# Kernel optimization log

Hardware: AMD Instinct MI355X
Metric: run time of the kernel (lower is better)

## Reference

```python
import jax, jax.numpy as jnp
from jax import lax
import numpy as np

B, CIN, NC, H, W = 8, 64, 4, 192, 192
TAU = 4.0
ALPHA = 2.0
LOSS_W = 0.5
OVERALL_W = 1.0
K = 3  # edge-extraction kernel size


def setup_inputs() -> dict:
    key = jax.random.key(0)
    k1, k2, k3, k4 = jax.random.split(key, 4)
    feat_student = jax.random.normal(k1, (B, CIN, H, W), jnp.float32)
    logits_teacher = jax.random.normal(k2, (B, NC, H, W), jnp.float32)
    lbl_idx = jax.random.randint(k3, (B, H, W), 0, NC)
    label = jax.nn.one_hot(lbl_idx, NC, axis=1, dtype=jnp.float32)  # (B,NC,H,W)
    # 1x1 conv projector params (kaiming fan_out-ish scale), bias zero-init per module
    W_proj = jax.random.normal(k4, (NC, CIN), jnp.float32) * (2.0 / CIN) ** 0.5
    b_proj = jnp.zeros((NC,), jnp.float32)
    return {"feat_student": feat_student, "logits_teacher": logits_teacher,
            "label": label, "W_proj": W_proj, "b_proj": b_proj}


def _edt(mask):
    """Exact Euclidean distance transform of a bool (H,W) mask: distance of each
    pixel to the nearest False pixel (0 at False pixels). Separable exact EDT:
    1D row distances, then min over rows of f^2 + dr^2."""
    h, w = mask.shape
    big = jnp.float32(h + w)  # > max possible true distance
    pos = jnp.arange(w, dtype=jnp.float32)
    zero = ~mask
    left = lax.cummax(jnp.where(zero, pos, -big), axis=1)            # nearest zero idx to the left
    right = lax.cummin(jnp.where(zero, pos, 2.0 * big), axis=1, reverse=True)
    f = jnp.minimum(jnp.minimum(pos - left, right - pos), big)       # (H,W) 1D row distance
    rr = jnp.arange(h, dtype=jnp.float32)
    dr2 = (rr[:, None] - rr[None, :]) ** 2                           # (H,H)
    d2 = jnp.min(f[None, :, :] ** 2 + dr2[:, :, None], axis=1)       # (H,W)
    return jnp.sqrt(d2)


def _distance_field(img):
    """img: (B,H,W) float. fg_dist + bg_dist per image; zeros if mask all-same
    (mirrors scipy distance_transform_edt loop)."""
    mask = img > 0.5

    def per_image(m):
        nontrivial = m.any() & ~m.all()
        return jnp.where(nontrivial, _edt(m) + _edt(~m), 0.0)

    return jax.vmap(per_image)(mask)


def _extract_edge(label):
    # per-channel 3x3 ones conv == sum pooling; edge where 0 < sum < K*K
    conv = lax.reduce_window(label, 0.0, lax.add, (1, 1, K, K), (1, 1, 1, 1),
                             [(0, 0), (0, 0), (K // 2, K // 2), (K // 2, K // 2)])
    return ((conv > 0) & (conv < K * K)).astype(jnp.float32)


def reference(feat_student, logits_teacher, label, W_proj, b_proj):
    # projector: 1x1 conv
    logits_s = jnp.einsum('bchw,kc->bkhw', feat_student, W_proj) + b_proj[None, :, None, None]

    # ---- BoundaryKD (ECKD) ----
    edge = _extract_edge(label)[:, 1:]              # drop background channel
    s = (logits_s[:, 1:] * edge) / TAU
    t = (logits_teacher[:, 1:] * edge) / TAU
    p = jax.nn.log_softmax(s, axis=1)
    q = jax.nn.softmax(t, axis=1)
    # F.kl_div(p, q, 'batchmean') = sum(q*(log q - p)) / B
    kl = jnp.sum(jax.scipy.special.xlogy(q, q) - q * p) / B
    bkd_loss = kl * TAU ** 2

    # ---- LogHausdorffDT (SRKD) ----
    probs = jax.nn.softmax(logits_s, axis=1)
    tgt = jax.nn.one_hot(jnp.argmax(logits_teacher, axis=1), NC, axis=1, dtype=probs.dtype)
    pf = probs[:, 1:]   # (B, NC-1, H, W)
    tf = tgt[:, 1:]
    losses = []
    for c in range(NC - 1):   # small fixed loop over foreground classes
        pdt = lax.stop_gradient(_distance_field(pf[:, c]))
        tdt = lax.stop_gradient(_distance_field(tf[:, c]))
        err = (pf[:, c] - tf[:, c]) ** 2
        losses.append(jnp.mean(err * (pdt ** ALPHA + tdt ** ALPHA)))
    hd_loss = jnp.log(jnp.mean(jnp.stack(losses)) + 1.0)

    return (bkd_loss * OVERALL_W * LOSS_W, hd_loss * OVERALL_W * (1.0 - LOSS_W))
```

## Files before the change

### kernel.cpp

```cpp
#include <hip/hip_runtime.h>
#include <math.h>

#define BB 8
#define HH 192
#define WW 192
#define HW (HH*WW)
#define NPIX (BB*HW)

#define WS_ERR_OFF   256
#define WS_MP_OFF    3539200
#define WS_MT_OFF    4423936
#define WS_FQ_OFF    5308672

typedef unsigned char  u8;
typedef unsigned short u16;

__global__ __launch_bounds__(256) void k_main(
    const float* __restrict__ feat, const float* __restrict__ teach,
    const float* __restrict__ label, const float* __restrict__ Wp,
    const float* __restrict__ bp,
    float* __restrict__ err, u8* __restrict__ mp, u8* __restrict__ mt,
    int* __restrict__ cntp, int* __restrict__ cntt,
    double* __restrict__ klsum)
{
    __shared__ float  Ws[256];
    __shared__ float  bs[4];
    __shared__ int    scp[3], sct[3];
    __shared__ double skl[4];
    const int tid = threadIdx.x;
    Ws[tid] = Wp[tid];
    if (tid < 4) bs[tid] = bp[tid];
    if (tid < 3) { scp[tid] = 0; sct[tid] = 0; }
    __syncthreads();

    const int pix0 = (blockIdx.x*256 + tid)*2;
    const int b    = pix0 / HW;
    const int rem  = pix0 - b*HW;
    const int h    = rem / WW;
    const int w    = rem - h*WW;

    float acc[4][2];
    #pragma unroll
    for (int k = 0; k < 4; ++k) { acc[k][0] = 0.0f; acc[k][1] = 0.0f; }

    const float* fb = feat + (size_t)b*64*HW + rem;
    #pragma unroll 8
    for (int c = 0; c < 64; ++c) {
        float2 v = *reinterpret_cast<const float2*>(fb + (size_t)c*HW);
        float w0 = Ws[c], w1 = Ws[64+c], w2 = Ws[128+c], w3 = Ws[192+c];
        acc[0][0] += v.x*w0; acc[0][1] += v.y*w0;
        acc[1][0] += v.x*w1; acc[1][1] += v.y*w1;
        acc[2][0] += v.x*w2; acc[2][1] += v.y*w2;
        acc[3][0] += v.x*w3; acc[3][1] += v.y*w3;
    }
    float ls[4][2];
    #pragma unroll
    for (int k = 0; k < 4; ++k) {
        ls[k][0] = acc[k][0] + bs[k];
        ls[k][1] = acc[k][1] + bs[k];
    }

    const float* tb = teach + (size_t)b*4*HW + rem;
    float2 T0 = *reinterpret_cast<const float2*>(tb);
    float2 T1 = *reinterpret_cast<const float2*>(tb + HW);
    float2 T2 = *reinterpret_cast<const float2*>(tb + 2*HW);
    float2 T3 = *reinterpret_cast<const float2*>(tb + 3*HW);
    float tch[4][2] = {{T0.x,T0.y},{T1.x,T1.y},{T2.x,T2.y},{T3.x,T3.y}};

    float conv[3][2] = {{0,0},{0,0},{0,0}};
    #pragma unroll
    for (int ch = 0; ch < 3; ++ch) {
        const float* lc = label + (size_t)b*4*HW + (size_t)(ch+1)*HW;
        #pragma unroll
        for (int dy = -1; dy <= 1; ++dy) {
            int h2 = h + dy;
            if (h2 < 0 || h2 >= HH) continue;
            const float* lr = lc + h2*WW + w;
            float2 lm = *reinterpret_cast<const float2*>(lr);
            float lL = (w > 0)    ? lr[-1] : 0.0f;
            float lR = (w+2 < WW) ? lr[2]  : 0.0f;
            conv[ch][0] += lL   + lm.x + lm.y;
            conv[ch][1] += lm.x + lm.y + lR;
        }
    }

    double klloc = 0.0;
    float ev[3][2];
    bool  bm_p[3][2], bm_t[3][2];

    #pragma unroll
    for (int px = 0; px < 2; ++px) {
        float l0 = ls[0][px], l1 = ls[1][px], l2 = ls[2][px], l3 = ls[3][px];
        float t0 = tch[0][px], t1 = tch[1][px], t2 = tch[2][px], t3 = tch[3][px];

        int am = 0; float bv = t0;
        if (t1 > bv) { bv = t1; am = 1; }
        if (t2 > bv) { bv = t2; am = 2; }
        if (t3 > bv) { bv = t3; am = 3; }

        float lsk[3] = {l1, l2, l3}, tk[3] = {t1, t2, t3};
        float sv[3], tv[3];
        #pragma unroll
        for (int k = 0; k < 3; ++k) {
            float cvv = conv[k][px];
            float e = (cvv > 0.0f && cvv < 9.0f) ? 0.25f : 0.0f;
            sv[k] = lsk[k]*e; tv[k] = tk[k]*e;
        }

        float msv = fmaxf(fmaxf(sv[0], sv[1]), sv[2]);
        float es0 = expf(sv[0]-msv), es1 = expf(sv[1]-msv), es2 = expf(sv[2]-msv);
        float lse_s = logf(es0 + es1 + es2);
        float mtv = fmaxf(fmaxf(tv[0], tv[1]), tv[2]);
        float eq0 = expf(tv[0]-mtv), eq1 = expf(tv[1]-mtv), eq2 = expf(tv[2]-mtv);
        float sumq = eq0 + eq1 + eq2;
        float lse_t = logf(sumq);
        float invq = 1.0f / sumq;
        float eqs[3] = {eq0, eq1, eq2};
        float klp = 0.0f;
        #pragma unroll
        for (int k = 0; k < 3; ++k) {
            float q   = eqs[k]*invq;
            float lnq = (tv[k]-mtv) - lse_t;
            float p   = (sv[k]-msv) - lse_s;
            klp += q*(lnq - p);
        }
        klloc += (double)klp;

        float m4 = fmaxf(fmaxf(l0, l1), fmaxf(l2, l3));
        float e0 = expf(l0-m4), e1 = expf(l1-m4), e2 = expf(l2-m4), e3 = expf(l3-m4);
        float inv4 = 1.0f / (e0 + e1 + e2 + e3);
        float pfv[3] = {e1*inv4, e2*inv4, e3*inv4};

        #pragma unroll
        for (int k = 0; k < 3; ++k) {
            float pf = pfv[k];
            bool  bt = (am == k+1);
            float tf = bt ? 1.0f : 0.0f;
            float dd = pf - tf;
            ev[k][px]   = dd*dd;
            bm_p[k][px] = pf > 0.5f;
            bm_t[k][px] = bt;
        }
    }

    #pragma unroll
    for (int k = 0; k < 3; ++k) {
        size_t o = (size_t)(b*3 + k)*HW + rem;
        *reinterpret_cast<float2*>(err + o) = make_float2(ev[k][0], ev[k][1]);
        *reinterpret_cast<uchar2*>(mp + o) =
            make_uchar2((u8)bm_p[k][0], (u8)bm_p[k][1]);
        *reinterpret_cast<uchar2*>(mt + o) =
            make_uchar2((u8)bm_t[k][0], (u8)bm_t[k][1]);
    }

    const int lane = tid & 63;
    #pragma unroll
    for (int k = 0; k < 3; ++k) {
        int cp = 0, ctv = 0;
        #pragma unroll
        for (int px = 0; px < 2; ++px) {
            cp  += __popcll(__ballot(bm_p[k][px]));
            ctv += __popcll(__ballot(bm_t[k][px]));
        }
        if (lane == 0) { atomicAdd(&scp[k], cp); atomicAdd(&sct[k], ctv); }
    }

    #pragma unroll
    for (int off = 32; off; off >>= 1) klloc += __shfl_down(klloc, off);
    if (lane == 0) skl[tid >> 6] = klloc;
    __syncthreads();
    if (tid == 0) atomicAdd(klsum, skl[0]+skl[1]+skl[2]+skl[3]);
    if (tid < 3) {
        atomicAdd(&cntp[b*3 + tid], scp[tid]);
        atomicAdd(&cntt[b*3 + tid], sct[tid]);
    }
}

__global__ __launch_bounds__(64) void k_rows(
    const u8* __restrict__ mp, const u8* __restrict__ mt,
    u16* __restrict__ fq)
{
    const int gid = blockIdx.x*64 + threadIdx.x;
    const int row = gid % 192;
    const int pol = (gid / 192) & 1;
    const int jc  = gid / 384;
    const int src = jc / 24;
    const int bc  = jc % 24;
    const u8* m = (src == 0 ? mp : mt) + (size_t)bc*HW + (size_t)row*WW;
    u16* frow = fq + ((size_t)jc*2 + pol)*HW + (size_t)row*WW;
    const unsigned zv = (unsigned)pol;

    unsigned wv[48];
    const uint4* m4 = reinterpret_cast<const uint4*>(m);
    #pragma unroll
    for (int j = 0; j < 12; ++j) {
        uint4 v = m4[j];
        wv[4*j] = v.x; wv[4*j+1] = v.y; wv[4*j+2] = v.z; wv[4*j+3] = v.w;
    }

    unsigned dle[48];
    int last = -384;
    #pragma unroll
    for (int c = 0; c < 192; ++c) {
        unsigned byte = (wv[c >> 2] >> ((c & 3)*8)) & 0xffu;
        if (byte == zv) last = c;
        unsigned enc = (unsigned)min(c - last, 255);
        if ((c & 3) == 0) dle[c >> 2] = enc;
        else              dle[c >> 2] |= enc << ((c & 3)*8);
    }

    int nxt = 768;
    unsigned fp0 = 0, fp1 = 0, fp2 = 0, fp3 = 0;
    #pragma unroll
    for (int c = 191; c >= 0; --c) {
        unsigned byte = (wv[c >> 2] >> ((c & 3)*8)) & 0xffu;
        if (byte == zv) nxt = c;
        int dl = (int)((dle[c >> 2] >> ((c & 3)*8)) & 0xffu);
        if (dl == 255) dl = 384;
        unsigned f = (unsigned)min(min(dl, nxt - c), 384);
        const int j = c & 7;
        const int half = j & 1;
        unsigned hv = half ? (f << 16) : f;
        switch (j >> 1) {
            case 0: if (half) fp0 = hv; else fp0 |= hv; break;
            case 1: if (half) fp1 = hv; else fp1 |= hv; break;
            case 2: if (half) fp2 = hv; else fp2 |= hv; break;
            case 3: if (half) fp3 = hv; else fp3 |= hv; break;
        }
        if (j == 0)
            *reinterpret_cast<uint4*>(frow + c) = make_uint4(fp0, fp1, fp2, fp3);
    }
}

__global__ __launch_bounds__(256) void k_cols(
    const u16* __restrict__ fq, const float* __restrict__ err,
    const u8* __restrict__ mp, const u8* __restrict__ mt,
    const int* __restrict__ cntp, const int* __restrict__ cntt,
    double* __restrict__ hdsum)
{
    __shared__ float  fl[2][192][16];
    __shared__ float  smax[4];
    __shared__ double shd[4];
    __shared__ float  sRmax;
    const int jc   = blockIdx.x / 12;
    const int ct   = blockIdx.x % 12;
    const int col0 = ct*16;
    const int src  = jc / 24;
    const int bc   = jc % 24;
    const int cnt  = (src == 0 ? cntp : cntt)[bc];
    if (cnt <= 0 || cnt >= HW) return;

    const int tid = threadIdx.x;
    const u16* fj = fq + (size_t)jc*2*HW + col0;
    for (int i = tid; i < 1536; i += 256) {
        int pol  = i / 768;
        int remi = i - pol*768;
        int rr   = remi >> 2;
        int grp  = (remi & 3)*4;
        uint2 v = *reinterpret_cast<const uint2*>(fj + (size_t)pol*HW + rr*WW + grp);
        float f0 = (float)(v.x & 0xffffu), f1 = (float)(v.x >> 16);
        float f2 = (float)(v.y & 0xffffu), f3 = (float)(v.y >> 16);
        fl[pol][rr][grp]   = f0*f0;
        fl[pol][rr][grp+1] = f1*f1;
        fl[pol][rr][grp+2] = f2*f2;
        fl[pol][rr][grp+3] = f3*f3;
    }
    __syncthreads();

    const int cc = tid & 15;
    const int r0 = tid >> 4;
    const u8*    mrow = (src == 0 ? mp : mt) + (size_t)bc*HW + col0 + cc;
    const float* ep   = err + (size_t)bc*HW + col0 + cc;

    int   pol_i[12];
    float ev[12];
    float localmax = 0.0f;
    #pragma unroll
    for (int i = 0; i < 12; ++i) {
        int r = r0 + 16*i;
        bool m1 = mrow[(size_t)r*WW] != 0;
        pol_i[i] = m1 ? 0 : 1;
        ev[i]    = ep[(size_t)r*WW];
        localmax = fmaxf(localmax, fl[pol_i[i]][r][cc]);
    }
    const int lane = tid & 63;
    #pragma unroll
    for (int off = 32; off; off >>= 1)
        localmax = fmaxf(localmax, __shfl_down(localmax, off));
    if (lane == 0) smax[tid >> 6] = localmax;
    __syncthreads();
    if (tid == 0) sRmax = fmaxf(fmaxf(smax[0], smax[1]), fmaxf(smax[2], smax[3]));
    __syncthreads();
    const int R = (int)ceilf(sqrtf(sRmax));

    double a = 0.0;
    #pragma unroll
    for (int i = 0; i < 12; ++i) {
        int r   = r0 + 16*i;
        int rlo = max(0, r - R);
        int rhi = min(191, r + R);
        const float* bp_ = &fl[pol_i[i]][0][cc];
        float d  = 3.0e38f;
        float dr = (float)(r - rlo);
        for (int rp = rlo; rp <= rhi; ++rp) {
            d = fminf(d, fmaf(dr, dr, bp_[(size_t)rp*16]));
            dr -= 1.0f;
        }
        a += (double)(ev[i]*d);
    }

    #pragma unroll
    for (int off = 32; off; off >>= 1) a += __shfl_down(a, off);
    if (lane == 0) shd[tid >> 6] = a;
    __syncthreads();
    if (tid == 0) atomicAdd(hdsum, shd[0]+shd[1]+shd[2]+shd[3]);
}

__global__ void k_final(const double* __restrict__ klsum,
                        const double* __restrict__ hdsum,
                        float* __restrict__ out)
{
    if (threadIdx.x == 0 && blockIdx.x == 0) {
        double kl = klsum[0] / (double)BB;
        out[0] = (float)(kl * 16.0 * 0.5);
        double meanl = hdsum[0] / (3.0 * (double)NPIX);
        out[1] = (float)(log(meanl + 1.0) * 0.5);
    }
}

extern "C" void kernel_launch(void* const* d_in, const int* in_sizes, int n_in,
                              void* d_out, int out_size, void* d_ws, size_t ws_size,
                              hipStream_t stream) {
    const float* feat  = (const float*)d_in[0];
    const float* teach = (const float*)d_in[1];
    const float* label = (const float*)d_in[2];
    const float* Wp    = (const float*)d_in[3];
    const float* bp    = (const float*)d_in[4];
    float* out = (float*)d_out;

    char* ws = (char*)d_ws;
    double* klsum = (double*)(ws);
    double* hdsum = (double*)(ws + 8);
    int*    cntp  = (int*)(ws + 16);
    int*    cntt  = (int*)(ws + 112);
    float*  err   = (float*)(ws + WS_ERR_OFF);
    u8*     mp    = (u8*)(ws + WS_MP_OFF);
    u8*     mt    = (u8*)(ws + WS_MT_OFF);
    u16*    fq    = (u16*)(ws + WS_FQ_OFF);

    hipMemsetAsync(ws, 0, 256, stream);
    k_main <<<NPIX/512, 256, 0, stream>>>(feat, teach, label, Wp, bp,
                                          err, mp, mt, cntp, cntt, klsum);
    k_rows <<<(48*2*192)/64, 64, 0, stream>>>(mp, mt, fq);
    k_cols <<<48*12, 256, 0, stream>>>(fq, err, mp, mt, cntp, cntt, hdsum);
    k_final<<<1, 1, 0, stream>>>(klsum, hdsum, out);
}
```

Before: 198.5 us.

## Parallelize EDT row scans with wave prefix-scans and per-pixel column search

The main kernel moves from two pixels per thread to one pixel per thread. The row-distance kernel switches from one serial thread per row to one wave per row, using shuffle prefix max/min scans. The column kernel drops its shared-memory tile per column strip and assigns one thread per pixel. Each thread bounds its column search by the wave-wide maximum of its own row distance and reads u16 values straight from global memory. Block partial sums replace the global atomic and are reduced in a wider final kernel. This exposes more parallelism, but column reads become uncached global loads and the search radius depends on the worst pixel in each wave.

```diff
diff --git a/kernel.cpp b/kernel.cpp
--- a/kernel.cpp
+++ b/kernel.cpp
@@ -6,11 +6,13 @@
 #define WW 192
 #define HW (HH*WW)
 #define NPIX (BB*HW)
+#define NBLK_COLS (48*HW/256)
 
 #define WS_ERR_OFF   256
 #define WS_MP_OFF    3539200
 #define WS_MT_OFF    4423936
 #define WS_FQ_OFF    5308672
+#define WS_PART_OFF  12386560
 
 typedef unsigned char  u8;
 typedef unsigned short u16;
@@ -33,41 +35,25 @@
     if (tid < 3) { scp[tid] = 0; sct[tid] = 0; }
     __syncthreads();
 
-    const int pix0 = (blockIdx.x*256 + tid)*2;
-    const int b    = pix0 / HW;
-    const int rem  = pix0 - b*HW;
-    const int h    = rem / WW;
-    const int w    = rem - h*WW;
-
-    float acc[4][2];
-    #pragma unroll
-    for (int k = 0; k < 4; ++k) { acc[k][0] = 0.0f; acc[k][1] = 0.0f; }
-
+    const int pix = blockIdx.x*256 + tid;
+    const int b   = pix / HW;
+    const int rem = pix - b*HW;
+    const int h   = rem / WW;
+    const int w   = rem - h*WW;
+
+    float a0 = 0.f, a1 = 0.f, a2 = 0.f, a3 = 0.f;
     const float* fb = feat + (size_t)b*64*HW + rem;
     #pragma unroll 8
     for (int c = 0; c < 64; ++c) {
-        float2 v = *reinterpret_cast<const float2*>(fb + (size_t)c*HW);
-        float w0 = Ws[c], w1 = Ws[64+c], w2 = Ws[128+c], w3 = Ws[192+c];
-        acc[0][0] += v.x*w0; acc[0][1] += v.y*w0;
-        acc[1][0] += v.x*w1; acc[1][1] += v.y*w1;
-        acc[2][0] += v.x*w2; acc[2][1] += v.y*w2;
-        acc[3][0] += v.x*w3; acc[3][1] += v.y*w3;
-    }
-    float ls[4][2];
-    #pragma unroll
-    for (int k = 0; k < 4; ++k) {
-        ls[k][0] = acc[k][0] + bs[k];
-        ls[k][1] = acc[k][1] + bs[k];
-    }
+        float v = fb[(size_t)c*HW];
+        a0 += v*Ws[c]; a1 += v*Ws[64+c]; a2 += v*Ws[128+c]; a3 += v*Ws[192+c];
+    }
+    const float l0 = a0 + bs[0], l1 = a1 + bs[1], l2 = a2 + bs[2], l3 = a3 + bs[3];
 
     const float* tb = teach + (size_t)b*4*HW + rem;
-    float2 T0 = *reinterpret_cast<const float2*>(tb);
-    float2 T1 = *reinterpret_cast<const float2*>(tb + HW);
-    float2 T2 = *reinterpret_cast<const float2*>(tb + 2*HW);
-    float2 T3 = *reinterpret_cast<const float2*>(tb + 3*HW);
-    float tch[4][2] = {{T0.x,T0.y},{T1.x,T1.y},{T2.x,T2.y},{T3.x,T3.y}};
-
-    float conv[3][2] = {{0,0},{0,0},{0,0}};
+    const float t0 = tb[0], t1 = tb[HW], t2 = tb[2*HW], t3 = tb[3*HW];
+
+    float conv[3] = {0.f, 0.f, 0.f};
     #pragma unroll
     for (int ch = 0; ch < 3; ++ch) {
         const float* lc = label + (size_t)b*4*HW + (size_t)(ch+1)*HW;
@@ -76,92 +62,70 @@
             int h2 = h + dy;
             if (h2 < 0 || h2 >= HH) continue;
             const float* lr = lc + h2*WW + w;
-            float2 lm = *reinterpret_cast<const float2*>(lr);
-            float lL = (w > 0)    ? lr[-1] : 0.0f;
-            float lR = (w+2 < WW) ? lr[2]  : 0.0f;
-            conv[ch][0] += lL   + lm.x + lm.y;
-            conv[ch][1] += lm.x + lm.y + lR;
+            float s = lr[0];
+            if (w > 0)      s += lr[-1];
+            if (w < WW-1)   s += lr[1];
+            conv[ch] += s;
         }
     }
 
-    double klloc = 0.0;
-    float ev[3][2];
-    bool  bm_p[3][2], bm_t[3][2];
-
-    #pragma unroll
-    for (int px = 0; px < 2; ++px) {
-        float l0 = ls[0][px], l1 = ls[1][px], l2 = ls[2][px], l3 = ls[3][px];
-        float t0 = tch[0][px], t1 = tch[1][px], t2 = tch[2][px], t3 = tch[3][px];
-
-        int am = 0; float bv = t0;
-        if (t1 > bv) { bv = t1; am = 1; }
-        if (t2 > bv) { bv = t2; am = 2; }
-        if (t3 > bv) { bv = t3; am = 3; }
-
-        float lsk[3] = {l1, l2, l3}, tk[3] = {t1, t2, t3};
-        float sv[3], tv[3];
-        #pragma unroll
-        for (int k = 0; k < 3; ++k) {
-            float cvv = conv[k][px];
-            float e = (cvv > 0.0f && cvv < 9.0f) ? 0.25f : 0.0f;
-            sv[k] = lsk[k]*e; tv[k] = tk[k]*e;
-        }
-
-        float msv = fmaxf(fmaxf(sv[0], sv[1]), sv[2]);
-        float es0 = expf(sv[0]-msv), es1 = expf(sv[1]-msv), es2 = expf(sv[2]-msv);
-        float lse_s = logf(es0 + es1 + es2);
-        float mtv = fmaxf(fmaxf(tv[0], tv[1]), tv[2]);
-        float eq0 = expf(tv[0]-mtv), eq1 = expf(tv[1]-mtv), eq2 = expf(tv[2]-mtv);
-        float sumq = eq0 + eq1 + eq2;
-        float lse_t = logf(sumq);
-        float invq = 1.0f / sumq;
-        float eqs[3] = {eq0, eq1, eq2};
-        float klp = 0.0f;
-        #pragma unroll
-        for (int k = 0; k < 3; ++k) {
-            float q   = eqs[k]*invq;
-            float lnq = (tv[k]-mtv) - lse_t;
-            float p   = (sv[k]-msv) - lse_s;
-            klp += q*(lnq - p);
-        }
-        klloc += (double)klp;
-
-        float m4 = fmaxf(fmaxf(l0, l1), fmaxf(l2, l3));
-        float e0 = expf(l0-m4), e1 = expf(l1-m4), e2 = expf(l2-m4), e3 = expf(l3-m4);
-        float inv4 = 1.0f / (e0 + e1 + e2 + e3);
-        float pfv[3] = {e1*inv4, e2*inv4, e3*inv4};
-
-        #pragma unroll
-        for (int k = 0; k < 3; ++k) {
-            float pf = pfv[k];
-            bool  bt = (am == k+1);
-            float tf = bt ? 1.0f : 0.0f;
-            float dd = pf - tf;
-            ev[k][px]   = dd*dd;
-            bm_p[k][px] = pf > 0.5f;
-            bm_t[k][px] = bt;
-        }
-    }
-
-    #pragma unroll
-    for (int k = 0; k < 3; ++k) {
+    int am = 0; float bv = t0;
+    if (t1 > bv) { bv = t1; am = 1; }
+    if (t2 > bv) { bv = t2; am = 2; }
+    if (t3 > bv) { bv = t3; am = 3; }
+
+    const float lsk[3] = {l1, l2, l3}, tk[3] = {t1, t2, t3};
+    float sv[3], tv[3];
+    #pragma unroll
+    for (int k = 0; k < 3; ++k) {
+        float e = (conv[k] > 0.0f && conv[k] < 9.0f) ? 0.25f : 0.0f;
+        sv[k] = lsk[k]*e; tv[k] = tk[k]*e;
+    }
+
+    float msv = fmaxf(fmaxf(sv[0], sv[1]), sv[2]);
+    float es0 = expf(sv[0]-msv), es1 = expf(sv[1]-msv), es2 = expf(sv[2]-msv);
+    float lse_s = logf(es0 + es1 + es2);
+    float mtv = fmaxf(fmaxf(tv[0], tv[1]), tv[2]);
+    float eq0 = expf(tv[0]-mtv), eq1 = expf(tv[1]-mtv), eq2 = expf(tv[2]-mtv);
+    float sumq = eq0 + eq1 + eq2;
+    float lse_t = logf(sumq);
+    float invq = 1.0f / sumq;
+    float eqs[3] = {eq0, eq1, eq2};
+    float klp = 0.0f;
+    #pragma unroll
+    for (int k = 0; k < 3; ++k) {
+        float q   = eqs[k]*invq;
+        float lnq = (tv[k]-mtv) - lse_t;
+        float p   = (sv[k]-msv) - lse_s;
+        klp += q*(lnq - p);
+    }
+    double klloc = (double)klp;
+
+    float m4 = fmaxf(fmaxf(l0, l1), fmaxf(l2, l3));
+    float e0 = expf(l0-m4), e1 = expf(l1-m4), e2 = expf(l2-m4), e3 = expf(l3-m4);
+    float inv4 = 1.0f / (e0 + e1 + e2 + e3);
+    float pfv[3] = {e1*inv4, e2*inv4, e3*inv4};
+
+    bool bm_p[3], bm_t[3];
+    #pragma unroll
+    for (int k = 0; k < 3; ++k) {
+        float pf = pfv[k];
+        bool  bt = (am == k+1);
+        float tf = bt ? 1.0f : 0.0f;
+        float dd = pf - tf;
         size_t o = (size_t)(b*3 + k)*HW + rem;
-        *reinterpret_cast<float2*>(err + o) = make_float2(ev[k][0], ev[k][1]);
-        *reinterpret_cast<uchar2*>(mp + o) =
-            make_uchar2((u8)bm_p[k][0], (u8)bm_p[k][1]);
-        *reinterpret_cast<uchar2*>(mt + o) =
-            make_uchar2((u8)bm_t[k][0], (u8)bm_t[k][1]);
-    }
-
-    const int lane = tid & 63;
-    #pragma unroll
-    for (int k = 0; k < 3; ++k) {
-        int cp = 0, ctv = 0;
-        #pragma unroll
-        for (int px = 0; px < 2; ++px) {
-            cp  += __popcll(__ballot(bm_p[k][px]));
-            ctv += __popcll(__ballot(bm_t[k][px]));
-        }
+        err[o] = dd*dd;
+        bm_p[k] = pf > 0.5f;
+        bm_t[k] = bt;
+        mp[o] = bm_p[k] ? 1 : 0;
+        mt[o] = bt ? 1 : 0;
+    }
+
+    const int lane = tid & 63;
+    #pragma unroll
+    for (int k = 0; k < 3; ++k) {
+        int cp  = __popcll(__ballot(bm_p[k]));
+        int ctv = __popcll(__ballot(bm_t[k]));
         if (lane == 0) { atomicAdd(&scp[k], cp); atomicAdd(&sct[k], ctv); }
     }
 
@@ -176,155 +140,128 @@
     }
 }
 
-__global__ __launch_bounds__(64) void k_rows(
+__global__ __launch_bounds__(256) void k_rows(
     const u8* __restrict__ mp, const u8* __restrict__ mt,
     u16* __restrict__ fq)
 {
-    const int gid = blockIdx.x*64 + threadIdx.x;
-    const int row = gid % 192;
-    const int pol = (gid / 192) & 1;
-    const int jc  = gid / 384;
-    const int src = jc / 24;
-    const int bc  = jc % 24;
+    const int tid  = threadIdx.x;
+    const int lane = tid & 63;
+    const int wid  = blockIdx.x*4 + (tid >> 6);
+    const int row  = wid % 192;
+    const int pol  = (wid / 192) & 1;
+    const int jc   = wid / 384;
+    const int src  = jc / 24;
+    const int bc   = jc % 24;
     const u8* m = (src == 0 ? mp : mt) + (size_t)bc*HW + (size_t)row*WW;
     u16* frow = fq + ((size_t)jc*2 + pol)*HW + (size_t)row*WW;
-    const unsigned zv = (unsigned)pol;
-
-    unsigned wv[48];
-    const uint4* m4 = reinterpret_cast<const uint4*>(m);
-    #pragma unroll
-    for (int j = 0; j < 12; ++j) {
-        uint4 v = m4[j];
-        wv[4*j] = v.x; wv[4*j+1] = v.y; wv[4*j+2] = v.z; wv[4*j+3] = v.w;
-    }
-
-    unsigned dle[48];
-    int last = -384;
-    #pragma unroll
-    for (int c = 0; c < 192; ++c) {
-        unsigned byte = (wv[c >> 2] >> ((c & 3)*8)) & 0xffu;
-        if (byte == zv) last = c;
-        unsigned enc = (unsigned)min(c - last, 255);
-        if ((c & 3) == 0) dle[c >> 2] = enc;
-        else              dle[c >> 2] |= enc << ((c & 3)*8);
-    }
-
-    int nxt = 768;
-    unsigned fp0 = 0, fp1 = 0, fp2 = 0, fp3 = 0;
-    #pragma unroll
-    for (int c = 191; c >= 0; --c) {
-        unsigned byte = (wv[c >> 2] >> ((c & 3)*8)) & 0xffu;
-        if (byte == zv) nxt = c;
-        int dl = (int)((dle[c >> 2] >> ((c & 3)*8)) & 0xffu);
-        if (dl == 255) dl = 384;
-        unsigned f = (unsigned)min(min(dl, nxt - c), 384);
-        const int j = c & 7;
-        const int half = j & 1;
-        unsigned hv = half ? (f << 16) : f;
-        switch (j >> 1) {
-            case 0: if (half) fp0 = hv; else fp0 |= hv; break;
-            case 1: if (half) fp1 = hv; else fp1 |= hv; break;
-            case 2: if (half) fp2 = hv; else fp2 |= hv; break;
-            case 3: if (half) fp3 = hv; else fp3 |= hv; break;
-        }
-        if (j == 0)
-            *reinterpret_cast<uint4*>(frow + c) = make_uint4(fp0, fp1, fp2, fp3);
-    }
+    const int zv = pol;
+
+    const int c0 = lane*3;
+    const int m0 = m[c0], m1 = m[c0+1], m2 = m[c0+2];
+
+    const int z0 = (m0 == zv) ? c0   : -384;
+    const int z1 = (m1 == zv) ? c0+1 : -384;
+    const int z2 = (m2 == zv) ? c0+2 : -384;
+    int s = max(z0, max(z1, z2));
+    #pragma unroll
+    for (int off = 1; off < 64; off <<= 1) {
+        int t = __shfl_up(s, off);
+        if (lane >= off) s = max(s, t);
+    }
+    int excl = __shfl_up(s, 1);
+    if (lane == 0) excl = -384;
+    const int L0 = max(excl, z0);
+    const int L1 = max(L0, z1);
+    const int L2 = max(L1, z2);
+
+    const int y0 = (m0 == zv) ? c0   : 768;
+    const int y1 = (m1 == zv) ? c0+1 : 768;
+    const int y2 = (m2 == zv) ? c0+2 : 768;
+    int s2 = min(y0, min(y1, y2));
+    #pragma unroll
+    for (int off = 1; off < 64; off <<= 1) {
+        int t = __shfl_down(s2, off);
+        if (lane < 64-off) s2 = min(s2, t);
+    }
+    int exclr = __shfl_down(s2, 1);
+    if (lane == 63) exclr = 768;
+    const int R2 = min(exclr, y2);
+    const int R1 = min(R2, y1);
+    const int R0 = min(R1, y0);
+
+    frow[c0]   = (u16)min(min(c0   - L0, R0 - c0  ), 384);
+    frow[c0+1] = (u16)min(min(c0+1 - L1, R1 - c0-1), 384);
+    frow[c0+2] = (u16)min(min(c0+2 - L2, R2 - c0-2), 384);
 }
 
 __global__ __launch_bounds__(256) void k_cols(
     const u16* __restrict__ fq, const float* __restrict__ err,
     const u8* __restrict__ mp, const u8* __restrict__ mt,
     const int* __restrict__ cntp, const int* __restrict__ cntt,
-    double* __restrict__ hdsum)
-{
-    __shared__ float  fl[2][192][16];
-    __shared__ float  smax[4];
+    double* __restrict__ partial)
+{
     __shared__ double shd[4];
-    __shared__ float  sRmax;
-    const int jc   = blockIdx.x / 12;
-    const int ct   = blockIdx.x % 12;
-    const int col0 = ct*16;
-    const int src  = jc / 24;
-    const int bc   = jc % 24;
-    const int cnt  = (src == 0 ? cntp : cntt)[bc];
-    if (cnt <= 0 || cnt >= HW) return;
-
     const int tid = threadIdx.x;
-    const u16* fj = fq + (size_t)jc*2*HW + col0;
-    for (int i = tid; i < 1536; i += 256) {
-        int pol  = i / 768;
-        int remi = i - pol*768;
-        int rr   = remi >> 2;
-        int grp  = (remi & 3)*4;
-        uint2 v = *reinterpret_cast<const uint2*>(fj + (size_t)pol*HW + rr*WW + grp);
-        float f0 = (float)(v.x & 0xffffu), f1 = (float)(v.x >> 16);
-        float f2 = (float)(v.y & 0xffffu), f3 = (float)(v.y >> 16);
-        fl[pol][rr][grp]   = f0*f0;
-        fl[pol][rr][grp+1] = f1*f1;
-        fl[pol][rr][grp+2] = f2*f2;
-        fl[pol][rr][grp+3] = f3*f3;
-    }
-    __syncthreads();
-
-    const int cc = tid & 15;
-    const int r0 = tid >> 4;
-    const u8*    mrow = (src == 0 ? mp : mt) + (size_t)bc*HW + col0 + cc;
-    const float* ep   = err + (size_t)bc*HW + col0 + cc;
-
-    int   pol_i[12];
-    float ev[12];
-    float localmax = 0.0f;
-    #pragma unroll
-    for (int i = 0; i < 12; ++i) {
-        int r = r0 + 16*i;
-        bool m1 = mrow[(size_t)r*WW] != 0;
-        pol_i[i] = m1 ? 0 : 1;
-        ev[i]    = ep[(size_t)r*WW];
-        localmax = fmaxf(localmax, fl[pol_i[i]][r][cc]);
-    }
-    const int lane = tid & 63;
-    #pragma unroll
-    for (int off = 32; off; off >>= 1)
-        localmax = fmaxf(localmax, __shfl_down(localmax, off));
-    if (lane == 0) smax[tid >> 6] = localmax;
-    __syncthreads();
-    if (tid == 0) sRmax = fmaxf(fmaxf(smax[0], smax[1]), fmaxf(smax[2], smax[3]));
-    __syncthreads();
-    const int R = (int)ceilf(sqrtf(sRmax));
+    const int gid = blockIdx.x*256 + tid;
+    const int jc  = gid / HW;
+    const int pix = gid - jc*HW;
+    const int r   = pix / WW;
+    const int col = pix - r*WW;
+    const int src = jc / 24;
+    const int bc  = jc % 24;
+    const int cnt = (src == 0 ? cntp : cntt)[bc];
 
     double a = 0.0;
-    #pragma unroll
-    for (int i = 0; i < 12; ++i) {
-        int r   = r0 + 16*i;
-        int rlo = max(0, r - R);
-        int rhi = min(191, r + R);
-        const float* bp_ = &fl[pol_i[i]][0][cc];
-        float d  = 3.0e38f;
+    if (cnt > 0 && cnt < HW) {
+        const u8* mb = (src == 0 ? mp : mt) + (size_t)bc*HW;
+        const int pol = mb[pix] ? 0 : 1;
+        const u16* fbase = fq + ((size_t)jc*2 + pol)*HW;
+        const float e   = err[(size_t)bc*HW + pix];
+        const int  fown = fbase[pix];
+
+        int Rw = fown;
+        #pragma unroll
+        for (int off = 32; off; off >>= 1) Rw = max(Rw, __shfl_xor(Rw, off));
+
+        const int rlo = max(0, r - Rw);
+        const int rhi = min(191, r + Rw);
+        float d  = (float)fown * (float)fown;
         float dr = (float)(r - rlo);
+        const u16* fp = fbase + col;
         for (int rp = rlo; rp <= rhi; ++rp) {
-            d = fminf(d, fmaf(dr, dr, bp_[(size_t)rp*16]));
+            float fv = (float)fp[(size_t)rp*WW];
+            d = fminf(d, fmaf(dr, dr, fv*fv));
             dr -= 1.0f;
         }
-        a += (double)(ev[i]*d);
-    }
-
+        a = (double)(e * d);
+    }
+
+    const int lane = tid & 63;
     #pragma unroll
     for (int off = 32; off; off >>= 1) a += __shfl_down(a, off);
     if (lane == 0) shd[tid >> 6] = a;
     __syncthreads();
-    if (tid == 0) atomicAdd(hdsum, shd[0]+shd[1]+shd[2]+shd[3]);
-}
-
-__global__ void k_final(const double* __restrict__ klsum,
-                        const double* __restrict__ hdsum,
-                        float* __restrict__ out)
-{
-    if (threadIdx.x == 0 && blockIdx.x == 0) {
+    if (tid == 0) partial[blockIdx.x] = shd[0]+shd[1]+shd[2]+shd[3];
+}
+
+__global__ __launch_bounds__(256) void k_final(
+    const double* __restrict__ klsum, const double* __restrict__ partial,
+    float* __restrict__ out)
+{
+    __shared__ double sm[4];
+    const int tid = threadIdx.x;
+    double a = 0.0;
+    for (int i = tid; i < NBLK_COLS; i += 256) a += partial[i];
+    const int lane = tid & 63;
+    #pragma unroll
+    for (int off = 32; off; off >>= 1) a += __shfl_down(a, off);
+    if (lane == 0) sm[tid >> 6] = a;
+    __syncthreads();
+    if (tid == 0) {
+        double hd = sm[0]+sm[1]+sm[2]+sm[3];
         double kl = klsum[0] / (double)BB;
         out[0] = (float)(kl * 16.0 * 0.5);
-        double meanl = hdsum[0] / (3.0 * (double)NPIX);
-        out[1] = (float)(log(meanl + 1.0) * 0.5);
+        out[1] = (float)(log(hd / (3.0*(double)NPIX) + 1.0) * 0.5);
     }
 }
 
@@ -339,19 +276,19 @@
     float* out = (float*)d_out;
 
     char* ws = (char*)d_ws;
-    double* klsum = (double*)(ws);
-    double* hdsum = (double*)(ws + 8);
-    int*    cntp  = (int*)(ws + 16);
-    int*    cntt  = (int*)(ws + 112);
-    float*  err   = (float*)(ws + WS_ERR_OFF);
-    u8*     mp    = (u8*)(ws + WS_MP_OFF);
-    u8*     mt    = (u8*)(ws + WS_MT_OFF);
-    u16*    fq    = (u16*)(ws + WS_FQ_OFF);
+    double* klsum   = (double*)(ws);
+    int*    cntp    = (int*)(ws + 16);
+    int*    cntt    = (int*)(ws + 112);
+    float*  err     = (float*)(ws + WS_ERR_OFF);
+    u8*     mp      = (u8*)(ws + WS_MP_OFF);
+    u8*     mt      = (u8*)(ws + WS_MT_OFF);
+    u16*    fq      = (u16*)(ws + WS_FQ_OFF);
+    double* partial = (double*)(ws + WS_PART_OFF);
 
     hipMemsetAsync(ws, 0, 256, stream);
-    k_main <<<NPIX/512, 256, 0, stream>>>(feat, teach, label, Wp, bp,
+    k_main <<<NPIX/256, 256, 0, stream>>>(feat, teach, label, Wp, bp,
                                           err, mp, mt, cntp, cntt, klsum);
-    k_rows <<<(48*2*192)/64, 64, 0, stream>>>(mp, mt, fq);
-    k_cols <<<48*12, 256, 0, stream>>>(fq, err, mp, mt, cntp, cntt, hdsum);
-    k_final<<<1, 1, 0, stream>>>(klsum, hdsum, out);
-}
+    k_rows <<<(48*2*192)/4, 256, 0, stream>>>(mp, mt, fq);
+    k_cols <<<NBLK_COLS, 256, 0, stream>>>(fq, err, mp, mt, cntp, cntt, partial);
+    k_final<<<1, 256, 0, stream>>>(klsum, partial, out);
+}
```

Result: no change. 196.7 us (-0.9%).
